# Optimization experiments

Measured on AMD Instinct MI355X. Metric: run time of the kernel, lower is better.

The kernel has to match this reference:

```python
import jax, jax.numpy as jnp
import numpy as np

N_USER, N_ARTICLE, N_CAT = 200000, 100000, 500
D, H, C, L = 64, 4, 16, 2
SIZES = {"user": N_USER, "article": N_ARTICLE, "category": N_CAT}
# (src_type, dst_type, n_edges) in HeteroConv dict order
EDGE_DEFS = [
    ("user", "article", 1000000),    # comments
    ("article", "user", 1000000),    # rev_comments
    ("user", "user", 500000),        # replied_to
    ("user", "user", 500000),        # interacts_with
    ("article", "category", 100000), # belongs_to
    ("category", "article", 100000), # has_article
    ("user", "category", 500000),    # interested_in
    ("category", "user", 500000),    # attracts
]


def setup_inputs() -> dict:
    key = jax.random.key(0)
    ks = jax.random.split(key, 32)
    inp = {
        "x_user": 0.1 * jax.random.normal(ks[0], (N_USER, D), jnp.float32),
        "x_article": 0.1 * jax.random.normal(ks[1], (N_ARTICLE, D), jnp.float32),
        "x_category": 0.1 * jax.random.normal(ks[2], (N_CAT, D), jnp.float32),
        "Wsrc": jax.random.normal(ks[3], (L, 8, D, D), jnp.float32) / jnp.sqrt(jnp.float32(D)),
        "Wdst": jax.random.normal(ks[4], (L, 8, D, D), jnp.float32) / jnp.sqrt(jnp.float32(D)),
        "att_src": 0.1 * jax.random.normal(ks[5], (L, 8, H, C), jnp.float32),
        "att_dst": 0.1 * jax.random.normal(ks[6], (L, 8, H, C), jnp.float32),
        "bias": jnp.zeros((L, 8, D), jnp.float32),
    }
    for t, (s, d, E) in enumerate(EDGE_DEFS):
        row = jax.random.randint(ks[8 + 2 * t], (E,), 0, SIZES[s], dtype=jnp.int32)
        col = jax.random.randint(ks[9 + 2 * t], (E,), 0, SIZES[d], dtype=jnp.int32)
        inp[f"ei{t}"] = jnp.stack([row, col])  # [2, E]
    return inp


def _gat(x_s, x_d, ei, Ws, Wd, a_s_w, a_d_w, b):
    """PyG GATConv((in,in), C, heads=H, add_self_loops=False), concat heads."""
    n_dst = x_d.shape[0]
    hs = (x_s @ Ws).reshape(-1, H, C)          # [Ns, H, C]
    hd = (x_d @ Wd).reshape(-1, H, C)          # [Nd, H, C]
    a_s = (hs * a_s_w).sum(-1)                 # [Ns, H]
    a_d = (hd * a_d_w).sum(-1)                 # [Nd, H]
    row, col = ei[0], ei[1]
    e = jax.nn.leaky_relu(a_s[row] + a_d[col], 0.2)  # [E, H]
    # numerically-stable segment softmax over edges grouped by destination
    m = jax.ops.segment_max(e, col, num_segments=n_dst)
    m = jnp.where(jnp.isfinite(m), m, jnp.float32(0.0))
    ex = jnp.exp(e - m[col])
    den = jax.ops.segment_sum(ex, col, num_segments=n_dst)
    w = ex / (den[col] + 1e-16)                # [E, H]
    out = jax.ops.segment_sum(hs[row] * w[:, :, None], col, num_segments=n_dst)
    return out.reshape(n_dst, H * C) + b


def _forward(x_user, x_article, x_category, Wsrc, Wdst, att_src, att_dst, bias, edges):
    x = {"user": x_user, "article": x_article, "category": x_category}
    all_u = [x["user"]]
    all_i = [x["article"]]
    for l in range(L):
        out = {k: jnp.zeros_like(v) for k, v in x.items()}
        for t, (s, d, _) in enumerate(EDGE_DEFS):  # HeteroConv aggr='sum'
            out[d] = out[d] + _gat(x[s], x[d], edges[t],
                                   Wsrc[l, t], Wdst[l, t],
                                   att_src[l, t], att_dst[l, t], bias[l, t])
        x = {k: jax.nn.leaky_relu(v, 0.01) for k, v in out.items()}  # dropout is identity in eval
        all_u.append(x["user"])
        all_i.append(x["article"])
    user_final = jnp.stack(all_u, 1).mean(1)
    item_final = jnp.stack(all_i, 1).mean(1)
    return user_final, item_final


def reference(x_user, x_article, x_category, Wsrc, Wdst, att_src, att_dst, bias,
              ei0, ei1, ei2, ei3, ei4, ei5, ei6, ei7):
    edges = [ei0, ei1, ei2, ei3, ei4, ei5, ei6, ei7]
    return _forward(x_user, x_article, x_category, Wsrc, Wdst, att_src, att_dst, bias, edges)
```

## Files before the change

kernel.cpp:

```cpp
#include <hip/hip_runtime.h>
#include <hip/hip_bf16.h>


static constexpr int kNUser = 200000;
static constexpr int kNArt  = 100000;
static constexpr int kNCat  = 500;
static constexpr size_t SZ_U = (size_t)kNUser * 64;
static constexpr size_t SZ_A = (size_t)kNArt * 64;
static constexpr size_t SZ_C = (size_t)kNCat * 64;
static constexpr size_t SZ_X = SZ_U + SZ_A + SZ_C;
static constexpr int CHUNK = 4096;


__global__ __launch_bounds__(256, 4) void k_transform(const float* __restrict__ x,
    const float* __restrict__ W, const float* __restrict__ att,
    float* __restrict__ hs, float* __restrict__ a_s, int Ns)
{
  __shared__ float sXt[64 * 68];
  __shared__ float sW[64 * 64];
  __shared__ float sAtt[64];
  int tid = threadIdx.x;
  int r0 = blockIdx.x * 64;

  {
    const float4* w4 = (const float4*)W;
    float4* s4 = (float4*)sW;
    #pragma unroll
    for (int i = 0; i < 4; ++i) s4[tid + 256 * i] = w4[tid + 256 * i];
  }
  if (tid < 64) sAtt[tid] = att[tid];
  {
    int r = tid >> 4, kq = tid & 15;
    #pragma unroll
    for (int rg = 0; rg < 4; ++rg) {
      int row = r0 + rg * 16 + r;
      float4 xv = make_float4(0.f, 0.f, 0.f, 0.f);
      if (row < Ns) xv = *(const float4*)(x + (size_t)row * 64 + kq * 4);
      sXt[(kq * 4 + 0) * 68 + rg * 16 + r] = xv.x;
      sXt[(kq * 4 + 1) * 68 + rg * 16 + r] = xv.y;
      sXt[(kq * 4 + 2) * 68 + rg * 16 + r] = xv.z;
      sXt[(kq * 4 + 3) * 68 + rg * 16 + r] = xv.w;
    }
  }
  __syncthreads();

  int c4 = tid & 15, r4 = tid >> 4;
  float acc[4][4];
  #pragma unroll
  for (int i = 0; i < 4; ++i)
    #pragma unroll
    for (int j = 0; j < 4; ++j) acc[i][j] = 0.f;

  #pragma unroll 16
  for (int k = 0; k < 64; ++k) {
    float4 xv = *(const float4*)&sXt[k * 68 + r4 * 4];
    float4 wv = *(const float4*)&sW[k * 64 + c4 * 4];
    const float* xf = &xv.x;
    const float* wf = &wv.x;
    #pragma unroll
    for (int i = 0; i < 4; ++i)
      #pragma unroll
      for (int j = 0; j < 4; ++j) acc[i][j] += xf[i] * wf[j];
  }

  float attv[4];
  #pragma unroll
  for (int j = 0; j < 4; ++j) attv[j] = sAtt[c4 * 4 + j];
  int h = c4 >> 2;
  #pragma unroll
  for (int i = 0; i < 4; ++i) {
    int row = r0 + r4 * 4 + i;
    bool ok = row < Ns;
    if (ok) *(float4*)(hs + (size_t)row * 64 + c4 * 4) =
        make_float4(acc[i][0], acc[i][1], acc[i][2], acc[i][3]);
    float p = acc[i][0] * attv[0] + acc[i][1] * attv[1] +
              acc[i][2] * attv[2] + acc[i][3] * attv[3];
    p += __shfl_xor(p, 1, 64);
    p += __shfl_xor(p, 2, 64);
    if ((c4 & 3) == 0 && ok) a_s[(size_t)row * 4 + h] = p;
  }
}

__global__ __launch_bounds__(256) void k_ad(const float* __restrict__ x,
    const float* __restrict__ Wd, const float* __restrict__ att,
    float* __restrict__ a_d, int Nd)
{
  __shared__ float sV[256];
  int tid = threadIdx.x;
  {
    int k = tid >> 2, h = tid & 3;
    float s = 0.f;
    #pragma unroll
    for (int c = 0; c < 16; ++c) s += Wd[k * 64 + h * 16 + c] * att[h * 16 + c];
    sV[k * 4 + h] = s;
  }
  __syncthreads();
  int n = blockIdx.x * 256 + tid;
  if (n >= Nd) return;
  const float4* x4 = (const float4*)(x + (size_t)n * 64);
  float a0 = 0.f, a1 = 0.f, a2 = 0.f, a3 = 0.f;
  #pragma unroll
  for (int k4 = 0; k4 < 16; ++k4) {
    float4 xv = x4[k4];
    const float* f = &xv.x;
    #pragma unroll
    for (int j = 0; j < 4; ++j) {
      int k = k4 * 4 + j;
      float xk = f[j];
      a0 += xk * sV[k * 4 + 0];
      a1 += xk * sV[k * 4 + 1];
      a2 += xk * sV[k * 4 + 2];
      a3 += xk * sV[k * 4 + 3];
    }
  }
  *(float4*)(a_d + (size_t)n * 4) = make_float4(a0, a1, a2, a3);
}


__global__ __launch_bounds__(256) void k_bhist(const int* __restrict__ col, int E,
    int nblk, int nbin, int shift, int* __restrict__ bh)
{
  __shared__ int h[1024];
  int tid = threadIdx.x;
  for (int j = tid; j < nbin; j += 256) h[j] = 0;
  __syncthreads();
  int b = blockIdx.x;
  int lo = b * CHUNK, hi = min(E, lo + CHUNK);
  for (int i = lo + tid; i < hi; i += 256) atomicAdd(&h[col[i] >> shift], 1);
  __syncthreads();
  for (int j = tid; j < nbin; j += 256) bh[j * nblk + b] = h[j];
}

__global__ __launch_bounds__(256) void k_s1(const int* __restrict__ a,
    int* __restrict__ bsum, int n)
{
  __shared__ int tmp[256];
  int t = threadIdx.x;
  int base = blockIdx.x * 4096 + t * 16;
  int s = 0;
  #pragma unroll
  for (int i = 0; i < 16; ++i) { int idx = base + i; if (idx < n) s += a[idx]; }
  tmp[t] = s;
  __syncthreads();
  for (int off = 128; off > 0; off >>= 1) {
    if (t < off) tmp[t] += tmp[t + off];
    __syncthreads();
  }
  if (t == 0) bsum[blockIdx.x] = tmp[0];
}

__global__ __launch_bounds__(1024) void k_s2(int* __restrict__ bsum, int nb) {
  __shared__ int tmp[1024];
  int t = threadIdx.x;
  int v = (t < nb) ? bsum[t] : 0;
  tmp[t] = v;
  __syncthreads();
  for (int off = 1; off < 1024; off <<= 1) {
    int u = (t >= off) ? tmp[t - off] : 0;
    __syncthreads();
    tmp[t] += u;
    __syncthreads();
  }
  if (t < nb) bsum[t] = tmp[t] - v;
}

__global__ __launch_bounds__(256) void k_s3(int* __restrict__ a,
    const int* __restrict__ bsum, int n)
{
  __shared__ int tw[256];
  int t = threadIdx.x;
  int base = blockIdx.x * 4096 + t * 16;
  int v[16];
  int s = 0;
  #pragma unroll
  for (int i = 0; i < 16; ++i) { int idx = base + i; v[i] = (idx < n) ? a[idx] : 0; s += v[i]; }
  tw[t] = s;
  __syncthreads();
  for (int off = 1; off < 256; off <<= 1) {
    int u = (t >= off) ? tw[t - off] : 0;
    __syncthreads();
    tw[t] += u;
    __syncthreads();
  }
  int excl = bsum[blockIdx.x] + tw[t] - s;
  #pragma unroll
  for (int i = 0; i < 16; ++i) {
    int idx = base + i;
    if (idx < n) { a[idx] = excl; excl += v[i]; }
  }
}

__global__ void k_binbase(const int* __restrict__ bh, int nblk, int nbin, int E,
                          int* __restrict__ binbase)
{
  int j = blockIdx.x * 256 + threadIdx.x;
  if (j < nbin) binbase[j] = bh[(size_t)j * nblk];
  if (j == nbin) binbase[nbin] = E;
}

__global__ __launch_bounds__(256) void k_bscat(const int* __restrict__ row,
    const int* __restrict__ col, int E, int nblk, int nbin, int shift,
    const int* __restrict__ bh,
    int* __restrict__ trow, int* __restrict__ tcol)
{
  __shared__ int cur[1024];
  int tid = threadIdx.x;
  int b = blockIdx.x;
  for (int j = tid; j < nbin; j += 256) cur[j] = bh[j * nblk + b];
  __syncthreads();
  int lo = b * CHUNK, hi = min(E, lo + CHUNK);
  for (int i = lo + tid; i < hi; i += 256) {
    int c = col[i];
    int p = atomicAdd(&cur[c >> shift], 1);
    trow[p] = row[i];
    if (tcol) tcol[p] = c;
  }
}

__global__ __launch_bounds__(256) void k_fine(const int* __restrict__ trow,
    const int* __restrict__ tcol, const int* __restrict__ binbase,
    int* __restrict__ rowptr, int* __restrict__ rows, int Nd, int nbin)
{
  __shared__ int h[256], sc[256], cur[256];
  int tid = threadIdx.x;
  int bin = blockIdx.x;
  int s = binbase[bin], e = binbase[bin + 1];
  h[tid] = 0;
  __syncthreads();
  for (int k = s + tid; k < e; k += 256) atomicAdd(&h[tcol[k] & 255], 1);
  __syncthreads();
  int own = h[tid];
  sc[tid] = own;
  __syncthreads();
  for (int off = 1; off < 256; off <<= 1) {
    int t = (tid >= off) ? sc[tid - off] : 0;
    __syncthreads();
    sc[tid] += t;
    __syncthreads();
  }
  int excl = sc[tid] - own;
  int dst = bin * 256 + tid;
  if (dst < Nd) rowptr[dst] = s + excl;
  cur[tid] = s + excl;
  if (bin == 0 && tid == 0) rowptr[Nd] = binbase[nbin];
  __syncthreads();
  for (int k = s + tid; k < e; k += 256) {
    int p = atomicAdd(&cur[tcol[k] & 255], 1);
    rows[p] = trow[k];
  }
}

__global__ void k_rp(const int* __restrict__ binbase, int* __restrict__ rowptr, int Nd) {
  int i = blockIdx.x * 256 + threadIdx.x;
  if (i <= Nd) rowptr[i] = binbase[i];
}


__global__ __launch_bounds__(256) void k_gather16(const int* __restrict__ rowptr,
    const int* __restrict__ rows, const float* __restrict__ a_s,
    const float* __restrict__ a_d, const float* __restrict__ hs,
    float* __restrict__ out, int Nd)
{
  int tid = threadIdx.x;
  int g = tid >> 4, lane = tid & 15, h = lane >> 2;
  int n = blockIdx.x * 16 + g;
  if (n >= Nd) return;
  float adh = a_d[(size_t)n * 4 + h];
  int start = rowptr[n], end = rowptr[n + 1];
  float m = -INFINITY, den = 0.f;
  float ax = 0.f, ay = 0.f, az = 0.f, aw = 0.f;
  for (int k = start; k < end; ++k) {
    int row = rows[k];
    float v = a_s[(size_t)row * 4 + h] + adh;
    v = v >= 0.f ? v : 0.2f * v;
    float mn = fmaxf(m, v);
    float c = __expf(m - mn);
    float p = __expf(v - mn);
    float4 hv = *(const float4*)(hs + (size_t)row * 64 + lane * 4);
    den = den * c + p;
    ax = ax * c + p * hv.x;
    ay = ay * c + p * hv.y;
    az = az * c + p * hv.z;
    aw = aw * c + p * hv.w;
    m = mn;
  }
  float inv = 1.f / (den + 1e-16f);
  float4* op = (float4*)(out + (size_t)n * 64) + lane;
  float4 prev = *op;
  prev.x += ax * inv; prev.y += ay * inv; prev.z += az * inv; prev.w += aw * inv;
  *op = prev;
}

__global__ __launch_bounds__(256) void k_gatherB(const int* __restrict__ rowptr,
    const int* __restrict__ rows, const float* __restrict__ a_s,
    const float* __restrict__ a_d, const float* __restrict__ hs,
    float* __restrict__ out)
{
  __shared__ float sm[64], sden[64], sacc[1024];
  int n = blockIdx.x;
  int tid = threadIdx.x;
  int sg = tid >> 4, lane = tid & 15, h = lane >> 2;
  float adh = a_d[(size_t)n * 4 + h];
  int start = rowptr[n], end = rowptr[n + 1];
  float m = -INFINITY, den = 0.f;
  float ax = 0.f, ay = 0.f, az = 0.f, aw = 0.f;
  for (int k = start + sg; k < end; k += 16) {
    int row = rows[k];
    float v = a_s[(size_t)row * 4 + h] + adh;
    v = v >= 0.f ? v : 0.2f * v;
    float mn = fmaxf(m, v);
    float c = __expf(m - mn);
    float p = __expf(v - mn);
    float4 hv = *(const float4*)(hs + (size_t)row * 64 + lane * 4);
    den = den * c + p;
    ax = ax * c + p * hv.x;
    ay = ay * c + p * hv.y;
    az = az * c + p * hv.z;
    aw = aw * c + p * hv.w;
    m = mn;
  }
  sacc[sg * 64 + lane * 4 + 0] = ax;
  sacc[sg * 64 + lane * 4 + 1] = ay;
  sacc[sg * 64 + lane * 4 + 2] = az;
  sacc[sg * 64 + lane * 4 + 3] = aw;
  if ((lane & 3) == 0) { sm[sg * 4 + h] = m; sden[sg * 4 + h] = den; }
  __syncthreads();
  if (tid < 64) {
    int hh = tid >> 4;
    float M = -INFINITY;
    #pragma unroll
    for (int g2 = 0; g2 < 16; ++g2) M = fmaxf(M, sm[g2 * 4 + hh]);
    if (M == -INFINITY) M = 0.f;
    float D = 0.f, A = 0.f;
    #pragma unroll
    for (int g2 = 0; g2 < 16; ++g2) {
      float mv = sm[g2 * 4 + hh];
      float c = (mv == -INFINITY) ? 0.f : __expf(mv - M);
      D += sden[g2 * 4 + hh] * c;
      A += sacc[g2 * 64 + tid] * c;
    }
    out[(size_t)n * 64 + tid] += A / (D + 1e-16f);
  }
}


__global__ void k_act(float* __restrict__ x, const float* __restrict__ b0,
                      const float* __restrict__ b1, const float* __restrict__ b2,
                      const float* __restrict__ b3, int nb, int n)
{
  int i = blockIdx.x * blockDim.x + threadIdx.x;
  if (i >= n) return;
  int d = i & 63;
  float bs = b0[d] + b1[d];
  if (nb == 4) bs += b2[d] + b3[d];
  float v = x[i] + bs;
  x[i] = v >= 0.f ? v : 0.01f * v;
}

__global__ void k_final(const float* __restrict__ x0, const float* __restrict__ x1,
                        const float* __restrict__ x2, float* __restrict__ out, int n)
{
  int i = blockIdx.x * blockDim.x + threadIdx.x;
  if (i < n) out[i] = (x0[i] + x1[i] + x2[i]) * (1.f / 3.f);
}


extern "C" void kernel_launch(void* const* d_in, const int* in_sizes, int n_in,
                              void* d_out, int out_size, void* d_ws, size_t ws_size,
                              hipStream_t stream)
{
  static const int ECNT[8] = {1000000, 1000000, 500000, 500000, 100000, 100000, 500000, 500000};
  static const int ESRC[8] = {0, 1, 0, 0, 1, 2, 0, 2};
  static const int EDST[8] = {1, 0, 0, 0, 2, 1, 2, 0};
  const int NSZ[3] = {kNUser, kNArt, kNCat};

  const float* x0[3] = {(const float*)d_in[0], (const float*)d_in[1], (const float*)d_in[2]};
  const float* Wsrc = (const float*)d_in[3];
  const float* Wdst = (const float*)d_in[4];
  const float* attS = (const float*)d_in[5];
  const float* attD = (const float*)d_in[6];
  const float* bias = (const float*)d_in[7];
  const int* ei[8];
  for (int t = 0; t < 8; ++t) ei[t] = (const int*)d_in[8 + t];

  float* ws = (float*)d_ws;
  size_t off = 0;
  auto alloc = [&](size_t nelem) { float* p = ws + off; off += nelem; return p; };
  float* xb0 = alloc(SZ_X);
  float* xb1 = alloc(SZ_X);
  float* hs  = alloc((size_t)kNUser * 64);
  float* a_s = alloc((size_t)kNUser * 4);
  float* a_d = alloc((size_t)kNUser * 4);
  int* rowptrA = (int*)alloc(1001008);
  int* rowsA   = (int*)alloc(4200000);
  int* tmp_row = (int*)alloc(1000000);
  int* tmp_col = (int*)alloc(1000000);
  int* blockhist = (int*)alloc(200704);
  int* binbase   = (int*)alloc(1032);
  int* bsum      = (int*)alloc(1024);

  int* rowptr_t[8]; int* rows_t[8];
  {
    size_t ro = 0, eo = 0;
    for (int t = 0; t < 8; ++t) {
      int Nd = NSZ[EDST[t]];
      rowptr_t[t] = rowptrA + ro; ro += (size_t)Nd + 1;
      rows_t[t]   = rowsA + eo;   eo += (size_t)ECNT[t];
    }
  }

  for (int t = 0; t < 8; ++t) {
    int Nd = NSZ[EDST[t]], E = ECNT[t];
    const int* row = ei[t];
    const int* col = ei[t] + E;
    int shift = (Nd <= 1024) ? 0 : 8;
    int nbin = ((Nd - 1) >> shift) + 1;
    int nblk = (E + CHUNK - 1) / CHUNK;
    int n = nbin * nblk;
    int nb2 = (n + 4095) / 4096;
    k_bhist<<<nblk, 256, 0, stream>>>(col, E, nblk, nbin, shift, blockhist);
    k_s1<<<nb2, 256, 0, stream>>>(blockhist, bsum, n);
    k_s2<<<1, 1024, 0, stream>>>(bsum, nb2);
    k_s3<<<nb2, 256, 0, stream>>>(blockhist, bsum, n);
    k_binbase<<<(nbin + 256) / 256, 256, 0, stream>>>(blockhist, nblk, nbin, E, binbase);
    if (shift == 0) {
      k_bscat<<<nblk, 256, 0, stream>>>(row, col, E, nblk, nbin, 0,
                                        blockhist, rows_t[t], nullptr);
      k_rp<<<(Nd + 256) / 256, 256, 0, stream>>>(binbase, rowptr_t[t], Nd);
    } else {
      k_bscat<<<nblk, 256, 0, stream>>>(row, col, E, nblk, nbin, 8,
                                        blockhist, tmp_row, tmp_col);
      k_fine<<<nbin, 256, 0, stream>>>(tmp_row, tmp_col, binbase,
                                       rowptr_t[t], rows_t[t], Nd, nbin);
    }
  }

  float* xb[2][3] = {{xb0, xb0 + SZ_U, xb0 + SZ_U + SZ_A},
                     {xb1, xb1 + SZ_U, xb1 + SZ_U + SZ_A}};
  const float* xcur[3] = {x0[0], x0[1], x0[2]};
  for (int l = 0; l < 2; ++l) {
    hipMemsetAsync(xb[l][0], 0, SZ_X * sizeof(float), stream);
    for (int t = 0; t < 8; ++t) {
      int s = ESRC[t], d = EDST[t];
      int Ns = NSZ[s], Nd = NSZ[d];
      const float* Ws = Wsrc + (size_t)(l * 8 + t) * 4096;
      const float* Wd = Wdst + (size_t)(l * 8 + t) * 4096;
      const float* aS = attS + (size_t)(l * 8 + t) * 64;
      const float* aD = attD + (size_t)(l * 8 + t) * 64;
      k_transform<<<(Ns + 63) / 64, 256, 0, stream>>>(xcur[s], Ws, aS, hs, a_s, Ns);
      k_ad<<<(Nd + 255) / 256, 256, 0, stream>>>(xcur[d], Wd, aD, a_d, Nd);
      if (Nd <= 512)
        k_gatherB<<<Nd, 256, 0, stream>>>(rowptr_t[t], rows_t[t], a_s, a_d, hs, xb[l][d]);
      else
        k_gather16<<<(Nd + 15) / 16, 256, 0, stream>>>(rowptr_t[t], rows_t[t], a_s, a_d, hs, xb[l][d], Nd);
    }
    const float* bl = bias + (size_t)l * 8 * 64;
    k_act<<<((int)SZ_U + 255) / 256, 256, 0, stream>>>(xb[l][0], bl + 64, bl + 128, bl + 192, bl + 448, 4, (int)SZ_U);
    k_act<<<((int)SZ_A + 255) / 256, 256, 0, stream>>>(xb[l][1], bl + 0,  bl + 320, bl, bl, 2, (int)SZ_A);
    k_act<<<((int)SZ_C + 255) / 256, 256, 0, stream>>>(xb[l][2], bl + 256, bl + 384, bl, bl, 2, (int)SZ_C);
    xcur[0] = xb[l][0]; xcur[1] = xb[l][1]; xcur[2] = xb[l][2];
  }
  k_final<<<((int)SZ_U + 255) / 256, 256, 0, stream>>>(x0[0], xb[0][0], xb[1][0], (float*)d_out, (int)SZ_U);
  k_final<<<((int)SZ_A + 255) / 256, 256, 0, stream>>>(x0[1], xb[0][1], xb[1][1], (float*)d_out + SZ_U, (int)SZ_A);
}
```

Baseline: 1.939 ms.

## Aggregate raw fp16 features then apply W after softmax, folding attention vectors into W

Folds W·att into per-node attention projections computed once per node type for all relations, and replaces the per-relation source transform with aggregation over fp16-packed raw source features followed by a per-destination 64x64 matmul. It also drops the online max-subtraction in the softmax. The intent is to remove the large hs write/read per relation, halve gather bandwidth, and share the attention dot products across relations. The cost is fp16 precision on the gathered features and possible exp overflow without the max shift, plus extra per-destination matmul work.

Result: slower. 2.069 ms (+6.7%).

```diff
diff --git a/kernel.cpp b/kernel.cpp
--- a/kernel.cpp
+++ b/kernel.cpp
@@ -1,5 +1,5 @@
 #include <hip/hip_runtime.h>
-#include <hip/hip_bf16.h>
+#include <hip/hip_fp16.h>
 
 
 static constexpr int kNUser = 200000;
@@ -11,109 +11,80 @@
 static constexpr size_t SZ_X = SZ_U + SZ_A + SZ_C;
 static constexpr int CHUNK = 4096;
 
-
-__global__ __launch_bounds__(256, 4) void k_transform(const float* __restrict__ x,
-    const float* __restrict__ W, const float* __restrict__ att,
-    float* __restrict__ hs, float* __restrict__ a_s, int Ns)
-{
-  __shared__ float sXt[64 * 68];
-  __shared__ float sW[64 * 64];
-  __shared__ float sAtt[64];
-  int tid = threadIdx.x;
-  int r0 = blockIdx.x * 64;
-
-  {
-    const float4* w4 = (const float4*)W;
-    float4* s4 = (float4*)sW;
+__device__ __forceinline__ uint32_t packh2(float a, float b) {
+  __half2 t = __floats2half2_rn(a, b);
+  return *reinterpret_cast<uint32_t*>(&t);
+}
+__device__ __forceinline__ float2 unpackh2(uint32_t u) {
+  __half2 t = *reinterpret_cast<__half2*>(&u);
+  return __half22float2(t);
+}
+
+__global__ void k_fold(const float* __restrict__ Wsrc, const float* __restrict__ Wdst,
+                       const float* __restrict__ attS, const float* __restrict__ attD,
+                       float* __restrict__ fold)
+{
+  int lt = blockIdx.x;
+  int tid = threadIdx.x;
+  int k = tid >> 2, h = tid & 3;
+  const float* Ws = Wsrc + (size_t)lt * 4096;
+  const float* Wd = Wdst + (size_t)lt * 4096;
+  const float* aS = attS + (size_t)lt * 64;
+  const float* aD = attD + (size_t)lt * 64;
+  float s = 0.f, d = 0.f;
+  #pragma unroll
+  for (int c = 0; c < 16; ++c) {
+    s += Ws[k * 64 + h * 16 + c] * aS[h * 16 + c];
+    d += Wd[k * 64 + h * 16 + c] * aD[h * 16 + c];
+  }
+  fold[((size_t)lt * 2 + 0) * 256 + tid] = s;
+  fold[((size_t)lt * 2 + 1) * 256 + tid] = d;
+}
+
+template <int NV>
+__global__ __launch_bounds__(256) void k_attn(const float* __restrict__ x,
+    uint4* __restrict__ xh, const float* __restrict__ fold,
+    int4 sa, int4 sb, float* __restrict__ aout, int Ns)
+{
+  __shared__ float sV[NV * 256];
+  int tid = threadIdx.x;
+  const int slots[8] = {sa.x, sa.y, sa.z, sa.w, sb.x, sb.y, sb.z, sb.w};
+  #pragma unroll
+  for (int v = 0; v < NV; ++v)
+    sV[v * 256 + tid] = fold[(size_t)slots[v] * 256 + tid];
+  __syncthreads();
+  int n = blockIdx.x * 256 + tid;
+  if (n >= Ns) return;
+  const float4* xp = (const float4*)(x + (size_t)n * 64);
+  float4 xr[16];
+  #pragma unroll
+  for (int q = 0; q < 16; ++q) xr[q] = xp[q];
+  uint4* dst = xh + (size_t)n * 8;
+  #pragma unroll
+  for (int q = 0; q < 8; ++q) {
+    uint4 u;
+    u.x = packh2(xr[2 * q].x, xr[2 * q].y);
+    u.y = packh2(xr[2 * q].z, xr[2 * q].w);
+    u.z = packh2(xr[2 * q + 1].x, xr[2 * q + 1].y);
+    u.w = packh2(xr[2 * q + 1].z, xr[2 * q + 1].w);
+    dst[q] = u;
+  }
+  #pragma unroll
+  for (int v = 0; v < NV; ++v) {
+    float a0 = 0.f, a1 = 0.f, a2 = 0.f, a3 = 0.f;
     #pragma unroll
-    for (int i = 0; i < 4; ++i) s4[tid + 256 * i] = w4[tid + 256 * i];
-  }
-  if (tid < 64) sAtt[tid] = att[tid];
-  {
-    int r = tid >> 4, kq = tid & 15;
-    #pragma unroll
-    for (int rg = 0; rg < 4; ++rg) {
-      int row = r0 + rg * 16 + r;
-      float4 xv = make_float4(0.f, 0.f, 0.f, 0.f);
-      if (row < Ns) xv = *(const float4*)(x + (size_t)row * 64 + kq * 4);
-      sXt[(kq * 4 + 0) * 68 + rg * 16 + r] = xv.x;
-      sXt[(kq * 4 + 1) * 68 + rg * 16 + r] = xv.y;
-      sXt[(kq * 4 + 2) * 68 + rg * 16 + r] = xv.z;
-      sXt[(kq * 4 + 3) * 68 + rg * 16 + r] = xv.w;
+    for (int q = 0; q < 16; ++q) {
+      const float* xf = &xr[q].x;
+      #pragma unroll
+      for (int j = 0; j < 4; ++j) {
+        int k = q * 4 + j;
+        float4 vv = *(const float4*)&sV[v * 256 + k * 4];
+        float xk = xf[j];
+        a0 += xk * vv.x; a1 += xk * vv.y; a2 += xk * vv.z; a3 += xk * vv.w;
+      }
     }
-  }
-  __syncthreads();
-
-  int c4 = tid & 15, r4 = tid >> 4;
-  float acc[4][4];
-  #pragma unroll
-  for (int i = 0; i < 4; ++i)
-    #pragma unroll
-    for (int j = 0; j < 4; ++j) acc[i][j] = 0.f;
-
-  #pragma unroll 16
-  for (int k = 0; k < 64; ++k) {
-    float4 xv = *(const float4*)&sXt[k * 68 + r4 * 4];
-    float4 wv = *(const float4*)&sW[k * 64 + c4 * 4];
-    const float* xf = &xv.x;
-    const float* wf = &wv.x;
-    #pragma unroll
-    for (int i = 0; i < 4; ++i)
-      #pragma unroll
-      for (int j = 0; j < 4; ++j) acc[i][j] += xf[i] * wf[j];
-  }
-
-  float attv[4];
-  #pragma unroll
-  for (int j = 0; j < 4; ++j) attv[j] = sAtt[c4 * 4 + j];
-  int h = c4 >> 2;
-  #pragma unroll
-  for (int i = 0; i < 4; ++i) {
-    int row = r0 + r4 * 4 + i;
-    bool ok = row < Ns;
-    if (ok) *(float4*)(hs + (size_t)row * 64 + c4 * 4) =
-        make_float4(acc[i][0], acc[i][1], acc[i][2], acc[i][3]);
-    float p = acc[i][0] * attv[0] + acc[i][1] * attv[1] +
-              acc[i][2] * attv[2] + acc[i][3] * attv[3];
-    p += __shfl_xor(p, 1, 64);
-    p += __shfl_xor(p, 2, 64);
-    if ((c4 & 3) == 0 && ok) a_s[(size_t)row * 4 + h] = p;
-  }
-}
-
-__global__ __launch_bounds__(256) void k_ad(const float* __restrict__ x,
-    const float* __restrict__ Wd, const float* __restrict__ att,
-    float* __restrict__ a_d, int Nd)
-{
-  __shared__ float sV[256];
-  int tid = threadIdx.x;
-  {
-    int k = tid >> 2, h = tid & 3;
-    float s = 0.f;
-    #pragma unroll
-    for (int c = 0; c < 16; ++c) s += Wd[k * 64 + h * 16 + c] * att[h * 16 + c];
-    sV[k * 4 + h] = s;
-  }
-  __syncthreads();
-  int n = blockIdx.x * 256 + tid;
-  if (n >= Nd) return;
-  const float4* x4 = (const float4*)(x + (size_t)n * 64);
-  float a0 = 0.f, a1 = 0.f, a2 = 0.f, a3 = 0.f;
-  #pragma unroll
-  for (int k4 = 0; k4 < 16; ++k4) {
-    float4 xv = x4[k4];
-    const float* f = &xv.x;
-    #pragma unroll
-    for (int j = 0; j < 4; ++j) {
-      int k = k4 * 4 + j;
-      float xk = f[j];
-      a0 += xk * sV[k * 4 + 0];
-      a1 += xk * sV[k * 4 + 1];
-      a2 += xk * sV[k * 4 + 2];
-      a3 += xk * sV[k * 4 + 3];
-    }
-  }
-  *(float4*)(a_d + (size_t)n * 4) = make_float4(a0, a1, a2, a3);
+    *(float4*)(aout + (size_t)n * (NV * 4) + v * 4) = make_float4(a0, a1, a2, a3);
+  }
 }
 
 
@@ -255,91 +226,123 @@
   if (i <= Nd) rowptr[i] = binbase[i];
 }
 
-
-__global__ __launch_bounds__(256) void k_gather16(const int* __restrict__ rowptr,
-    const int* __restrict__ rows, const float* __restrict__ a_s,
-    const float* __restrict__ a_d, const float* __restrict__ hs,
-    float* __restrict__ out, int Nd)
-{
-  int tid = threadIdx.x;
-  int g = tid >> 4, lane = tid & 15, h = lane >> 2;
+__global__ __launch_bounds__(256) void k_gat16(const int* __restrict__ rowptr,
+    const int* __restrict__ rows, const float* __restrict__ aS, int sS,
+    const float* __restrict__ aD, int sD, const uint32_t* __restrict__ xh,
+    const float* __restrict__ W, float* __restrict__ out, int Nd)
+{
+  __shared__ float sW[64 * 64];
+  __shared__ float sAgg[16][260];
+  int tid = threadIdx.x;
+  {
+    const float4* w4 = (const float4*)W;
+    float4* s4 = (float4*)sW;
+    #pragma unroll
+    for (int i = 0; i < 4; ++i) s4[tid + 256 * i] = w4[tid + 256 * i];
+  }
+  int g = tid >> 4, l = tid & 15, h = l & 3;
   int n = blockIdx.x * 16 + g;
-  if (n >= Nd) return;
-  float adh = a_d[(size_t)n * 4 + h];
+  float acc[4][4] = {{0.f,0.f,0.f,0.f},{0.f,0.f,0.f,0.f},{0.f,0.f,0.f,0.f},{0.f,0.f,0.f,0.f}};
+  float den[4] = {0.f, 0.f, 0.f, 0.f};
+  if (n < Nd) {
+    float adh = aD[(size_t)n * sD + h];
+    int start = rowptr[n], end = rowptr[n + 1];
+    for (int k = start; k < end; ++k) {
+      int row = rows[k];
+      float v = aS[(size_t)row * sS + h] + adh;
+      v = v >= 0.f ? v : 0.2f * v;
+      float p0 = __expf(v);
+      float p1 = __shfl_xor(p0, 1);
+      float p2 = __shfl_xor(p0, 2);
+      float p3 = __shfl_xor(p0, 3);
+      uint2 xr = *(const uint2*)(xh + (size_t)row * 32 + l * 2);
+      float2 x01 = unpackh2(xr.x);
+      float2 x23 = unpackh2(xr.y);
+      den[0] += p0; den[1] += p1; den[2] += p2; den[3] += p3;
+      acc[0][0] += p0 * x01.x; acc[0][1] += p0 * x01.y; acc[0][2] += p0 * x23.x; acc[0][3] += p0 * x23.y;
+      acc[1][0] += p1 * x01.x; acc[1][1] += p1 * x01.y; acc[1][2] += p1 * x23.x; acc[1][3] += p1 * x23.y;
+      acc[2][0] += p2 * x01.x; acc[2][1] += p2 * x01.y; acc[2][2] += p2 * x23.x; acc[2][3] += p2 * x23.y;
+      acc[3][0] += p3 * x01.x; acc[3][1] += p3 * x01.y; acc[3][2] += p3 * x23.x; acc[3][3] += p3 * x23.y;
+    }
+  }
+  #pragma unroll
+  for (int m = 0; m < 4; ++m) {
+    float inv = 1.f / (den[m] + 1e-16f);
+    *(float4*)&sAgg[g][(h ^ m) * 64 + l * 4] = make_float4(
+        acc[m][0] * inv, acc[m][1] * inv, acc[m][2] * inv, acc[m][3] * inv);
+  }
+  __syncthreads();
+  int c4 = tid & 15, hh = c4 >> 2;
+  float r0 = 0.f, r1 = 0.f, r2 = 0.f, r3 = 0.f;
+  #pragma unroll 8
+  for (int k = 0; k < 64; ++k) {
+    float a = sAgg[g][hh * 64 + k];
+    float4 wv = *(const float4*)&sW[k * 64 + c4 * 4];
+    r0 += a * wv.x; r1 += a * wv.y; r2 += a * wv.z; r3 += a * wv.w;
+  }
+  if (n < Nd) {
+    float4* op = (float4*)(out + (size_t)n * 64) + c4;
+    float4 pv = *op;
+    pv.x += r0; pv.y += r1; pv.z += r2; pv.w += r3;
+    *op = pv;
+  }
+}
+
+__global__ __launch_bounds__(256) void k_gatB(const int* __restrict__ rowptr,
+    const int* __restrict__ rows, const float* __restrict__ aS, int sS,
+    const float* __restrict__ aD, int sD, const uint32_t* __restrict__ xh,
+    const float* __restrict__ W, float* __restrict__ out)
+{
+  __shared__ float sAgg[16][260];
+  __shared__ float sDen[16][4];
+  __shared__ float sRes[256];
+  int n = blockIdx.x;
+  int tid = threadIdx.x;
+  int g = tid >> 4, l = tid & 15, h = l & 3;
+  float adh = aD[(size_t)n * sD + h];
   int start = rowptr[n], end = rowptr[n + 1];
-  float m = -INFINITY, den = 0.f;
-  float ax = 0.f, ay = 0.f, az = 0.f, aw = 0.f;
-  for (int k = start; k < end; ++k) {
+  float acc[4][4] = {{0.f,0.f,0.f,0.f},{0.f,0.f,0.f,0.f},{0.f,0.f,0.f,0.f},{0.f,0.f,0.f,0.f}};
+  float den[4] = {0.f, 0.f, 0.f, 0.f};
+  for (int k = start + g; k < end; k += 16) {
     int row = rows[k];
-    float v = a_s[(size_t)row * 4 + h] + adh;
+    float v = aS[(size_t)row * sS + h] + adh;
     v = v >= 0.f ? v : 0.2f * v;
-    float mn = fmaxf(m, v);
-    float c = __expf(m - mn);
-    float p = __expf(v - mn);
-    float4 hv = *(const float4*)(hs + (size_t)row * 64 + lane * 4);
-    den = den * c + p;
-    ax = ax * c + p * hv.x;
-    ay = ay * c + p * hv.y;
-    az = az * c + p * hv.z;
-    aw = aw * c + p * hv.w;
-    m = mn;
-  }
-  float inv = 1.f / (den + 1e-16f);
-  float4* op = (float4*)(out + (size_t)n * 64) + lane;
-  float4 prev = *op;
-  prev.x += ax * inv; prev.y += ay * inv; prev.z += az * inv; prev.w += aw * inv;
-  *op = prev;
-}
-
-__global__ __launch_bounds__(256) void k_gatherB(const int* __restrict__ rowptr,
-    const int* __restrict__ rows, const float* __restrict__ a_s,
-    const float* __restrict__ a_d, const float* __restrict__ hs,
-    float* __restrict__ out)
-{
-  __shared__ float sm[64], sden[64], sacc[1024];
-  int n = blockIdx.x;
-  int tid = threadIdx.x;
-  int sg = tid >> 4, lane = tid & 15, h = lane >> 2;
-  float adh = a_d[(size_t)n * 4 + h];
-  int start = rowptr[n], end = rowptr[n + 1];
-  float m = -INFINITY, den = 0.f;
-  float ax = 0.f, ay = 0.f, az = 0.f, aw = 0.f;
-  for (int k = start + sg; k < end; k += 16) {
-    int row = rows[k];
-    float v = a_s[(size_t)row * 4 + h] + adh;
-    v = v >= 0.f ? v : 0.2f * v;
-    float mn = fmaxf(m, v);
-    float c = __expf(m - mn);
-    float p = __expf(v - mn);
-    float4 hv = *(const float4*)(hs + (size_t)row * 64 + lane * 4);
-    den = den * c + p;
-    ax = ax * c + p * hv.x;
-    ay = ay * c + p * hv.y;
-    az = az * c + p * hv.z;
-    aw = aw * c + p * hv.w;
-    m = mn;
-  }
-  sacc[sg * 64 + lane * 4 + 0] = ax;
-  sacc[sg * 64 + lane * 4 + 1] = ay;
-  sacc[sg * 64 + lane * 4 + 2] = az;
-  sacc[sg * 64 + lane * 4 + 3] = aw;
-  if ((lane & 3) == 0) { sm[sg * 4 + h] = m; sden[sg * 4 + h] = den; }
+    float p0 = __expf(v);
+    float p1 = __shfl_xor(p0, 1);
+    float p2 = __shfl_xor(p0, 2);
+    float p3 = __shfl_xor(p0, 3);
+    uint2 xr = *(const uint2*)(xh + (size_t)row * 32 + l * 2);
+    float2 x01 = unpackh2(xr.x);
+    float2 x23 = unpackh2(xr.y);
+    den[0] += p0; den[1] += p1; den[2] += p2; den[3] += p3;
+    acc[0][0] += p0 * x01.x; acc[0][1] += p0 * x01.y; acc[0][2] += p0 * x23.x; acc[0][3] += p0 * x23.y;
+    acc[1][0] += p1 * x01.x; acc[1][1] += p1 * x01.y; acc[1][2] += p1 * x23.x; acc[1][3] += p1 * x23.y;
+    acc[2][0] += p2 * x01.x; acc[2][1] += p2 * x01.y; acc[2][2] += p2 * x23.x; acc[2][3] += p2 * x23.y;
+    acc[3][0] += p3 * x01.x; acc[3][1] += p3 * x01.y; acc[3][2] += p3 * x23.x; acc[3][3] += p3 * x23.y;
+  }
+  #pragma unroll
+  for (int m = 0; m < 4; ++m)
+    *(float4*)&sAgg[g][(h ^ m) * 64 + l * 4] =
+        make_float4(acc[m][0], acc[m][1], acc[m][2], acc[m][3]);
+  if (l == 0) {
+    sDen[g][0] = den[0]; sDen[g][1] = den[1]; sDen[g][2] = den[2]; sDen[g][3] = den[3];
+  }
+  __syncthreads();
+  float A = 0.f;
+  #pragma unroll
+  for (int gg = 0; gg < 16; ++gg) A += sAgg[gg][tid];
+  int hh = tid >> 6;
+  float D = 0.f;
+  #pragma unroll
+  for (int gg = 0; gg < 16; ++gg) D += sDen[gg][hh];
+  sRes[tid] = A / (D + 1e-16f);
   __syncthreads();
   if (tid < 64) {
-    int hh = tid >> 4;
-    float M = -INFINITY;
-    #pragma unroll
-    for (int g2 = 0; g2 < 16; ++g2) M = fmaxf(M, sm[g2 * 4 + hh]);
-    if (M == -INFINITY) M = 0.f;
-    float D = 0.f, A = 0.f;
-    #pragma unroll
-    for (int g2 = 0; g2 < 16; ++g2) {
-      float mv = sm[g2 * 4 + hh];
-      float c = (mv == -INFINITY) ? 0.f : __expf(mv - M);
-      D += sden[g2 * 4 + hh] * c;
-      A += sacc[g2 * 64 + tid] * c;
-    }
-    out[(size_t)n * 64 + tid] += A / (D + 1e-16f);
+    int hc = tid >> 4;
+    float r = 0.f;
+    #pragma unroll 8
+    for (int k = 0; k < 64; ++k) r += sRes[hc * 64 + k] * W[k * 64 + tid];
+    out[(size_t)n * 64 + tid] += r;
   }
 }
 
@@ -388,9 +391,11 @@
   auto alloc = [&](size_t nelem) { float* p = ws + off; off += nelem; return p; };
   float* xb0 = alloc(SZ_X);
   float* xb1 = alloc(SZ_X);
-  float* hs  = alloc((size_t)kNUser * 64);
-  float* a_s = alloc((size_t)kNUser * 4);
-  float* a_d = alloc((size_t)kNUser * 4);
+  float* xhf = alloc(SZ_X / 2);
+  float* aU  = alloc((size_t)kNUser * 32);
+  float* aA  = alloc((size_t)kNArt * 16);
+  float* aC  = alloc((size_t)kNCat * 16);
+  float* fold = alloc(16 * 2 * 256);
   int* rowptrA = (int*)alloc(1001008);
   int* rowsA   = (int*)alloc(4200000);
   int* tmp_row = (int*)alloc(1000000);
@@ -398,6 +403,11 @@
   int* blockhist = (int*)alloc(200704);
   int* binbase   = (int*)alloc(1032);
   int* bsum      = (int*)alloc(1024);
+
+  uint32_t* xh32 = (uint32_t*)xhf;
+  uint32_t* xh_u = xh32;
+  uint32_t* xh_a = xh32 + (size_t)kNUser * 32;
+  uint32_t* xh_c = xh_a + (size_t)kNArt * 32;
 
   int* rowptr_t[8]; int* rows_t[8];
   {
@@ -408,6 +418,14 @@
       rows_t[t]   = rowsA + eo;   eo += (size_t)ECNT[t];
     }
   }
+
+  float* aSp[8] = {aU + 0, aA + 0, aU + 4, aU + 8, aA + 4, aC + 0, aU + 12, aC + 4};
+  int    sSs[8] = {32, 16, 32, 32, 16, 16, 32, 16};
+  float* aDp[8] = {aA + 8, aU + 16, aU + 20, aU + 24, aC + 8, aA + 12, aC + 12, aU + 28};
+  int    sDs[8] = {16, 32, 32, 32, 16, 16, 16, 32};
+  const uint32_t* xhp[8] = {xh_u, xh_a, xh_u, xh_u, xh_a, xh_c, xh_u, xh_c};
+
+  k_fold<<<16, 256, 0, stream>>>(Wsrc, Wdst, attS, attD, fold);
 
   for (int t = 0; t < 8; ++t) {
     int Nd = NSZ[EDST[t]], E = ECNT[t];
@@ -440,19 +458,24 @@
   const float* xcur[3] = {x0[0], x0[1], x0[2]};
   for (int l = 0; l < 2; ++l) {
     hipMemsetAsync(xb[l][0], 0, SZ_X * sizeof(float), stream);
+    auto F = [&](int t, int sd) { return (l * 8 + t) * 2 + sd; };
+    int4 ua = make_int4(F(0, 0), F(2, 0), F(3, 0), F(6, 0));
+    int4 ub = make_int4(F(1, 1), F(2, 1), F(3, 1), F(7, 1));
+    int4 aa = make_int4(F(1, 0), F(4, 0), F(0, 1), F(5, 1));
+    int4 ca = make_int4(F(5, 0), F(7, 0), F(4, 1), F(6, 1));
+    k_attn<8><<<(kNUser + 255) / 256, 256, 0, stream>>>(xcur[0], (uint4*)xh_u, fold, ua, ub, aU, kNUser);
+    k_attn<4><<<(kNArt + 255) / 256, 256, 0, stream>>>(xcur[1], (uint4*)xh_a, fold, aa, aa, aA, kNArt);
+    k_attn<4><<<(kNCat + 255) / 256, 256, 0, stream>>>(xcur[2], (uint4*)xh_c, fold, ca, ca, aC, kNCat);
     for (int t = 0; t < 8; ++t) {
-      int s = ESRC[t], d = EDST[t];
-      int Ns = NSZ[s], Nd = NSZ[d];
-      const float* Ws = Wsrc + (size_t)(l * 8 + t) * 4096;
-      const float* Wd = Wdst + (size_t)(l * 8 + t) * 4096;
-      const float* aS = attS + (size_t)(l * 8 + t) * 64;
-      const float* aD = attD + (size_t)(l * 8 + t) * 64;
-      k_transform<<<(Ns + 63) / 64, 256, 0, stream>>>(xcur[s], Ws, aS, hs, a_s, Ns);
-      k_ad<<<(Nd + 255) / 256, 256, 0, stream>>>(xcur[d], Wd, aD, a_d, Nd);
+      int d = EDST[t];
+      int Nd = NSZ[d];
+      const float* Wt = Wsrc + (size_t)(l * 8 + t) * 4096;
       if (Nd <= 512)
-        k_gatherB<<<Nd, 256, 0, stream>>>(rowptr_t[t], rows_t[t], a_s, a_d, hs, xb[l][d]);
+        k_gatB<<<Nd, 256, 0, stream>>>(rowptr_t[t], rows_t[t], aSp[t], sSs[t],
+                                       aDp[t], sDs[t], xhp[t], Wt, xb[l][d]);
       else
-        k_gather16<<<(Nd + 15) / 16, 256, 0, stream>>>(rowptr_t[t], rows_t[t], a_s, a_d, hs, xb[l][d], Nd);
+        k_gat16<<<(Nd + 15) / 16, 256, 0, stream>>>(rowptr_t[t], rows_t[t], aSp[t], sSs[t],
+                                                    aDp[t], sDs[t], xhp[t], Wt, xb[l][d], Nd);
     }
     const float* bl = bias + (size_t)l * 8 * 64;
     k_act<<<((int)SZ_U + 255) / 256, 256, 0, stream>>>(xb[l][0], bl + 64, bl + 128, bl + 192, bl + 448, 4, (int)SZ_U);
```
